# Performance work log

Measured on AMD Instinct MI355X. Metric: run time of the kernel, lower is better.

The kernel has to match this reference:

```python
import jax, jax.numpy as jnp
import numpy as np
jax.config.update("jax_enable_x64", True)

HASH_PRIMES = [2654435761, 2246822519, 3266489917, 2028178513, 1220703125, 1610612741, 805306457, 402653189, 3674653429, 2860486313, 1073676287, 2971215073, 1500450271, 3267000013, 2654435789, 4049292737, 2246822531, 3266489927, 2028178519, 1220703133, 1610612743, 805306459, 402653191, 3674653433]
NUM_TABLES = 32
BUCKETS = 4096
VOCAB = 1024
BYTE_DIM = 256
EMBED_PER_TABLE = 8
HIDDEN = 512
N_BLOCKS = 3  # num_layers - 1
BATCH, SEQ = 32, 2048

def _generate_skip_patterns(num_tables):
    patterns = []
    for offset in range(1, min(num_tables // 4 + 1, 9)):
        patterns.append((offset,))
    pairs = [(1,2),(2,3),(3,4),(1,3),(2,4),(1,4),(1,5),(2,5),(3,5),(1,6),(2,6),(1,7)]
    for p in pairs:
        if len(patterns) >= num_tables:
            break
        patterns.append(p)
    trigrams = [(1,2,3),(1,2,4),(1,3,5),(2,3,4),(1,2,5),(1,3,4),(2,4,6),(1,4,7)]
    for t in trigrams:
        if len(patterns) >= num_tables:
            break
        patterns.append(t)
    offset = 8
    while len(patterns) < num_tables:
        patterns.append((1, offset))
        offset += 1
    return tuple(patterns[:num_tables])

SKIP_PATTERNS = _generate_skip_patterns(NUM_TABLES)

def _soft_hash(tokens, table_idx):
    # tokens: [B,S] int64. Faithful to torch: h = h ^ (shifted*prime);
    # h2 = h ^ ((h*prime2) >> 16)  (python precedence: * > >> > ^)
    B, S = tokens.shape
    pattern = SKIP_PATTERNS[table_idx]
    h = jnp.zeros((B, S), dtype=jnp.int64)
    for k, offset in enumerate(pattern):
        prime = HASH_PRIMES[(table_idx * 3 + k) % len(HASH_PRIMES)]
        shifted = jnp.zeros_like(tokens)
        if offset < S:
            shifted = shifted.at[:, offset:].set(tokens[:, :S - offset])
        h = h ^ (shifted * jnp.int64(prime))
    idx_lo = h % BUCKETS
    sp = HASH_PRIMES[(table_idx * 3 + len(pattern)) % len(HASH_PRIMES)]
    h2 = h ^ ((h * jnp.int64(sp)) >> 16)
    idx_hi = h2 % BUCKETS
    frac = (((h >> 3) & 255).astype(jnp.float32) / 255.0) * 0.4
    return idx_lo, idx_hi, frac

def setup_inputs() -> dict:
    key = jax.random.key(0)
    ks = jax.random.split(key, 8)
    chars = jax.random.randint(ks[0], (BATCH, SEQ), 0, VOCAB, dtype=jnp.int64)
    byte_embed = jax.random.normal(ks[1], (VOCAB, BYTE_DIM), dtype=jnp.float32)
    hash_tables = 0.02 * jax.random.normal(ks[2], (NUM_TABLES, BUCKETS, EMBED_PER_TABLE), dtype=jnp.float32)
    s_in = float(np.sqrt(6.0 / (HIDDEN + HIDDEN)))
    w_in = jax.random.uniform(ks[3], (HIDDEN, HIDDEN), jnp.float32, -s_in, s_in)
    b_in = jnp.zeros((HIDDEN,), jnp.float32)
    mlp_ws = jax.random.uniform(ks[4], (N_BLOCKS, HIDDEN, HIDDEN), jnp.float32, -s_in, s_in)
    mlp_bs = jnp.zeros((N_BLOCKS, HIDDEN), jnp.float32)
    s_out = float(np.sqrt(6.0 / (HIDDEN + VOCAB)))
    w_out = jax.random.uniform(ks[5], (VOCAB, HIDDEN), jnp.float32, -s_out, s_out)
    b_out = jnp.zeros((VOCAB,), jnp.float32)
    return {"chars": chars, "byte_embed": byte_embed, "hash_tables": hash_tables,
            "w_in": w_in, "b_in": b_in, "mlp_ws": mlp_ws, "mlp_bs": mlp_bs,
            "w_out": w_out, "b_out": b_out}

def reference(chars, byte_embed, hash_tables, w_in, b_in, mlp_ws, mlp_bs, w_out, b_out):
    # chars: [B,S] int64 -> logits [B,S,V]
    parts = [byte_embed[chars]]  # [B,S,256]
    for i in range(NUM_TABLES):
        idx_lo, idx_hi, frac = _soft_hash(chars, i)
        tab = hash_tables[i]                      # [BUCKETS, 8]
        frac = frac[..., None]                    # [B,S,1]
        emb = tab[idx_lo] * (1.0 - frac) + tab[idx_hi] * frac
        parts.append(emb)
    features = jnp.concatenate(parts, axis=-1)    # [B,S,512]
    h = jax.nn.relu(features @ w_in.T + b_in)
    for j in range(N_BLOCKS):
        # ResidualBlock: relu(linear(x)) + x (no layernorm/dropout in config)
        h = jax.nn.relu(h @ mlp_ws[j].T + mlp_bs[j]) + h
    logits = h @ w_out.T + b_out                  # [B,S,VOCAB]
    return logits
```

## Files before the change

### kernel.cpp

```cpp
#include <hip/hip_runtime.h>
#include <cstdint>
#include <cstddef>

typedef unsigned short u16;
typedef __attribute__((ext_vector_type(8))) short short8;
typedef __attribute__((ext_vector_type(4))) float f32x4;

#define NTOK 65536
#define HID 512
#define NVOCAB 1024

__device__ __forceinline__ u16 f2bf(float f) {
  union { float f; uint32_t u; } v; v.f = f;
  uint32_t r = (v.u + 0x7FFFu + ((v.u >> 16) & 1u)) >> 16;
  return (u16)r;
}
__device__ __forceinline__ float bf2f(u16 b) {
  union { uint32_t u; float f; } v; v.u = ((uint32_t)b) << 16;
  return v.f;
}

__constant__ uint32_t P24[24] = {
  2654435761u, 2246822519u, 3266489917u, 2028178513u, 1220703125u,
  1610612741u, 805306457u, 402653189u, 3674653429u, 2860486313u,
  1073676287u, 2971215073u, 1500450271u, 3267000013u, 2654435789u,
  4049292737u, 2246822531u, 3266489927u, 2028178519u, 1220703133u,
  1610612743u, 805306459u, 402653191u, 3674653433u};
__constant__ unsigned char OFFS[32][3] = {
  {1,0,0},{2,0,0},{3,0,0},{4,0,0},{5,0,0},{6,0,0},{7,0,0},{8,0,0},
  {1,2,0},{2,3,0},{3,4,0},{1,3,0},{2,4,0},{1,4,0},{1,5,0},{2,5,0},
  {3,5,0},{1,6,0},{2,6,0},{1,7,0},
  {1,2,3},{1,2,4},{1,3,5},{2,3,4},{1,2,5},{1,3,4},{2,4,6},{1,4,7},
  {1,8,0},{1,9,0},{1,10,0},{1,11,0}};
__constant__ unsigned char PLEN[32] = {
  1,1,1,1,1,1,1,1, 2,2,2,2,2,2,2,2,2,2,2,2, 3,3,3,3,3,3,3,3, 2,2,2,2};

__global__ __launch_bounds__(256) void pack_w(
    const float* __restrict__ w_in, const float* __restrict__ mlp_ws,
    const float* __restrict__ w_out, u16* __restrict__ Wp)
{
  const int gid  = blockIdx.x * 256 + threadIdx.x;
  const int L    = gid >> 15;
  const int c    = gid & 32767;
  const int lane = c & 63;
  const int ni   = (c >> 6) & 3;
  const int kk   = (c >> 8) & 15;
  const int w    = c >> 12;
  const float* base =
      (L == 0) ? w_in :
      (L <= 3) ? mlp_ws + (size_t)(L - 1) * 262144 :
                 w_out  + (size_t)(L - 4) * 262144;
  const int row = (w << 6) + (ni << 4) + (lane & 15);
  const int col = (kk << 5) + ((lane >> 4) << 3);
  const float* s = base + (size_t)row * 512 + col;
  float4 f0 = ((const float4*)s)[0];
  float4 f1 = ((const float4*)s)[1];
  short8 o;
  o[0]=(short)f2bf(f0.x); o[1]=(short)f2bf(f0.y); o[2]=(short)f2bf(f0.z); o[3]=(short)f2bf(f0.w);
  o[4]=(short)f2bf(f1.x); o[5]=(short)f2bf(f1.y); o[6]=(short)f2bf(f1.z); o[7]=(short)f2bf(f1.w);
  *(short8*)(Wp + (size_t)gid * 8) = o;
}

__global__ __launch_bounds__(512, 4)
void fused_all(const int* __restrict__ chars, const float* __restrict__ byte_embed,
               const float* __restrict__ hash_tables, const u16* __restrict__ Wp,
               const float* __restrict__ bIn, const float* __restrict__ bMlp,
               const float* __restrict__ bOut, float* __restrict__ out)
{
  __shared__ __align__(16) u16 hbuf[64 * 512];
  __shared__ int cbuf[96];
  const int tid  = threadIdx.x;
  const int w    = tid >> 6;
  const int lane = tid & 63;
  const int g    = lane >> 4;
  const int lr   = lane & 15;
  const size_t tok0 = (size_t)blockIdx.x << 6;
  const int swz = (lr & 7) << 3;

  if (tid < 96) {
    long long gi = (long long)tok0 - 32 + tid;
    if (gi < 0) gi = 0;
    cbuf[tid] = chars[gi];
  }
  __syncthreads();

  {
    const int sub = tid & 31;
    const int tl  = tid >> 5;
    const int pl  = (int)PLEN[sub];

    auto issue = [&](int tr, float4& g0, float4& g1, float4& g2,
                     float4& g3, float4& g4, float4& g5, float& fr) {
      const size_t t = tok0 + tr;
      const int pos = (int)(t & 2047);
      const int c = cbuf[32 + tr];
      long long hv = 0;
      #pragma unroll
      for (int k = 0; k < 3; ++k) {
        if (k < pl) {
          const int off = (int)OFFS[sub][k];
          const long long tok = (pos >= off) ? (long long)cbuf[32 + tr - off] : 0ll;
          hv ^= tok * (long long)P24[(3 * sub + k) % 24];
        }
      }
      const int idx_lo = (int)(hv & 4095);
      const long long sp = (long long)P24[(3 * sub + pl) % 24];
      const long long prod = (long long)((unsigned long long)hv * (unsigned long long)sp);
      const int idx_hi = (int)((hv ^ (prod >> 16)) & 4095);
      fr = ((float)(int)((hv >> 3) & 255) / 255.0f) * 0.4f;
      const float* plo = hash_tables + (((size_t)sub << 12) + (size_t)idx_lo) * 8;
      const float* phi = hash_tables + (((size_t)sub << 12) + (size_t)idx_hi) * 8;
      const float* pby = byte_embed + ((size_t)c << 8) + (sub << 3);
      g0 = ((const float4*)plo)[0]; g1 = ((const float4*)plo)[1];
      g2 = ((const float4*)phi)[0]; g3 = ((const float4*)phi)[1];
      g4 = ((const float4*)pby)[0]; g5 = ((const float4*)pby)[1];
    };
    auto consume = [&](int tr, float4 g0, float4 g1, float4 g2,
                       float4 g3, float4 g4, float4 g5, float fr) {
      const int sw = (tr & 7) << 3;
      short8 ob;
      ob[0]=(short)f2bf(g4.x); ob[1]=(short)f2bf(g4.y); ob[2]=(short)f2bf(g4.z); ob[3]=(short)f2bf(g4.w);
      ob[4]=(short)f2bf(g5.x); ob[5]=(short)f2bf(g5.y); ob[6]=(short)f2bf(g5.z); ob[7]=(short)f2bf(g5.w);
      *(short8*)&hbuf[(tr << 9) + ((sub << 3) ^ sw)] = ob;
      const float om = 1.0f - fr;
      short8 oh;
      oh[0]=(short)f2bf(g0.x*om + g2.x*fr); oh[1]=(short)f2bf(g0.y*om + g2.y*fr);
      oh[2]=(short)f2bf(g0.z*om + g2.z*fr); oh[3]=(short)f2bf(g0.w*om + g2.w*fr);
      oh[4]=(short)f2bf(g1.x*om + g3.x*fr); oh[5]=(short)f2bf(g1.y*om + g3.y*fr);
      oh[6]=(short)f2bf(g1.z*om + g3.z*fr); oh[7]=(short)f2bf(g1.w*om + g3.w*fr);
      *(short8*)&hbuf[(tr << 9) + ((256 + (sub << 3)) ^ sw)] = oh;
    };

    float4 A0, A1, A2, A3, A4, A5; float frA;
    float4 B0, B1, B2, B3, B4, B5; float frB;
    float4 C0, C1, C2, C3, C4, C5; float frC;
    issue(tl,      A0, A1, A2, A3, A4, A5, frA);
    issue(16 + tl, B0, B1, B2, B3, B4, B5, frB);
    issue(32 + tl, C0, C1, C2, C3, C4, C5, frC);
    consume(tl,      A0, A1, A2, A3, A4, A5, frA);
    issue(48 + tl,   A0, A1, A2, A3, A4, A5, frA);
    consume(16 + tl, B0, B1, B2, B3, B4, B5, frB);
    consume(32 + tl, C0, C1, C2, C3, C4, C5, frC);
    consume(48 + tl, A0, A1, A2, A3, A4, A5, frA);
  }
  __syncthreads();

  f32x4 acc[4][4];

  auto gemm = [&](int L) {
    #pragma unroll
    for (int ni = 0; ni < 4; ++ni)
      #pragma unroll
      for (int ti = 0; ti < 4; ++ti) acc[ni][ti] = (f32x4){0.f, 0.f, 0.f, 0.f};
    const u16* Wl = Wp + (size_t)L * 262144 + (w << 15) + (lane << 3);
    #pragma unroll
    for (int kk = 0; kk < 16; ++kk) {
      short8 Wf[4], hf[4];
      #pragma unroll
      for (int ni = 0; ni < 4; ++ni)
        Wf[ni] = *(const short8*)(Wl + (kk << 11) + (ni << 9));
      const int kb = ((kk << 5) + (g << 3)) ^ swz;
      #pragma unroll
      for (int ti = 0; ti < 4; ++ti)
        hf[ti] = *(const short8*)&hbuf[(((ti << 4) + lr) << 9) + kb];
      __builtin_amdgcn_s_setprio(1);
      #pragma unroll
      for (int ni = 0; ni < 4; ++ni)
        #pragma unroll
        for (int ti = 0; ti < 4; ++ti)
          acc[ni][ti] = __builtin_amdgcn_mfma_f32_16x16x32_bf16(Wf[ni], hf[ti], acc[ni][ti], 0, 0, 0);
      __builtin_amdgcn_s_setprio(0);
    }
  };

  auto epi_h = [&](const float* __restrict__ bias, bool resid) {
    __syncthreads();
    #pragma unroll
    for (int ni = 0; ni < 4; ++ni) {
      const int nb = (w << 6) + (ni << 4) + (g << 2);
      const float4 b4 = *(const float4*)(bias + nb);
      #pragma unroll
      for (int ti = 0; ti < 4; ++ti) {
        const int t = (ti << 4) + lr;
        u16* p = &hbuf[(t << 9) + (nb ^ swz)];
        float v0 = fmaxf(acc[ni][ti][0] + b4.x, 0.f);
        float v1 = fmaxf(acc[ni][ti][1] + b4.y, 0.f);
        float v2 = fmaxf(acc[ni][ti][2] + b4.z, 0.f);
        float v3 = fmaxf(acc[ni][ti][3] + b4.w, 0.f);
        if (resid) {
          const uint2 r2 = *(const uint2*)p;
          v0 += bf2f((u16)(r2.x & 0xffffu)); v1 += bf2f((u16)(r2.x >> 16));
          v2 += bf2f((u16)(r2.y & 0xffffu)); v3 += bf2f((u16)(r2.y >> 16));
        }
        uint2 o;
        o.x = (uint32_t)f2bf(v0) | ((uint32_t)f2bf(v1) << 16);
        o.y = (uint32_t)f2bf(v2) | ((uint32_t)f2bf(v3) << 16);
        *(uint2*)p = o;
      }
    }
    __syncthreads();
  };

  auto epi_out = [&](const float* __restrict__ bias, int vb) {
    #pragma unroll
    for (int ni = 0; ni < 4; ++ni) {
      const int nb = (w << 6) + (ni << 4) + (g << 2);
      const float4 b4 = *(const float4*)(bias + nb);
      #pragma unroll
      for (int ti = 0; ti < 4; ++ti) {
        const int t = (ti << 4) + lr;
        f32x4 o;
        o[0] = acc[ni][ti][0] + b4.x;
        o[1] = acc[ni][ti][1] + b4.y;
        o[2] = acc[ni][ti][2] + b4.z;
        o[3] = acc[ni][ti][3] + b4.w;
        __builtin_nontemporal_store(o, (f32x4*)(out + (tok0 + t) * NVOCAB + vb + nb));
      }
    }
  };

  gemm(0); epi_h(bIn, false);
  gemm(1); epi_h(bMlp,        true);
  gemm(2); epi_h(bMlp + 512,  true);
  gemm(3); epi_h(bMlp + 1024, true);
  gemm(4); epi_out(bOut,       0);
  gemm(5); epi_out(bOut + 512, 512);
}

extern "C" void kernel_launch(void* const* d_in, const int* in_sizes, int n_in,
                              void* d_out, int out_size, void* d_ws, size_t ws_size,
                              hipStream_t stream) {
  const int*   chars      = (const int*)  d_in[0];
  const float* byte_embed = (const float*)d_in[1];
  const float* hash_tabs  = (const float*)d_in[2];
  const float* w_in       = (const float*)d_in[3];
  const float* b_in       = (const float*)d_in[4];
  const float* mlp_ws     = (const float*)d_in[5];
  const float* mlp_bs     = (const float*)d_in[6];
  const float* w_out      = (const float*)d_in[7];
  const float* b_out      = (const float*)d_in[8];

  u16* Wp = (u16*)d_ws;

  pack_w<<<dim3(768), dim3(256), 0, stream>>>(w_in, mlp_ws, w_out, Wp);

  fused_all<<<dim3(NTOK / 64), dim3(512), 0, stream>>>(
      chars, byte_embed, hash_tabs, Wp, b_in, mlp_bs, b_out, (float*)d_out);
}
```

Baseline: 489.9 us.

## Switch GEMMs from 16x16x32 to 32x32x16 bf16 MFMA tiles

Replaces the 4x4 grid of 16x16x32 MFMAs per wave with a 2x2 grid of 32x32x16 MFMAs, and repacks the weights and reworks the LDS activation reads and epilogue indexing to match the new fragment layout. Each K step now issues fewer LDS and global fragment loads for the same output tile, and the larger MFMA gives better operand reuse. The trade-off is more K iterations with fewer instructions each, and a new swizzle and epilogue mapping that must line up exactly with the 32x32 accumulator layout.

```diff
diff --git a/kernel.cpp b/kernel.cpp
--- a/kernel.cpp
+++ b/kernel.cpp
@@ -5,6 +5,7 @@
 typedef unsigned short u16;
 typedef __attribute__((ext_vector_type(8))) short short8;
 typedef __attribute__((ext_vector_type(4))) float f32x4;
+typedef __attribute__((ext_vector_type(16))) float f32x16;
 
 #define NTOK 65536
 #define HID 512
@@ -43,15 +44,15 @@
   const int L    = gid >> 15;
   const int c    = gid & 32767;
   const int lane = c & 63;
-  const int ni   = (c >> 6) & 3;
-  const int kk   = (c >> 8) & 15;
+  const int ni   = (c >> 6) & 1;
+  const int kc   = (c >> 7) & 31;
   const int w    = c >> 12;
   const float* base =
       (L == 0) ? w_in :
       (L <= 3) ? mlp_ws + (size_t)(L - 1) * 262144 :
                  w_out  + (size_t)(L - 4) * 262144;
-  const int row = (w << 6) + (ni << 4) + (lane & 15);
-  const int col = (kk << 5) + ((lane >> 4) << 3);
+  const int row = (w << 6) + (ni << 5) + (lane & 31);
+  const int col = (kc << 4) + ((lane >> 5) << 3);
   const float* s = base + (size_t)row * 512 + col;
   float4 f0 = ((const float4*)s)[0];
   float4 f1 = ((const float4*)s)[1];
@@ -72,10 +73,10 @@
   const int tid  = threadIdx.x;
   const int w    = tid >> 6;
   const int lane = tid & 63;
-  const int g    = lane >> 4;
-  const int lr   = lane & 15;
+  const int tb   = lane & 31;
+  const int g2   = lane >> 5;
+  const int sx7  = lane & 7;
   const size_t tok0 = (size_t)blockIdx.x << 6;
-  const int swz = (lr & 7) << 3;
 
   if (tid < 96) {
     long long gi = (long long)tok0 - 32 + tid;
@@ -89,7 +90,7 @@
     const int tl  = tid >> 5;
     const int pl  = (int)PLEN[sub];
 
-    auto issue = [&](int tr, float4& g0, float4& g1, float4& g2,
+    auto issue = [&](int tr, float4& g0, float4& g1, float4& g2_,
                      float4& g3, float4& g4, float4& g5, float& fr) {
       const size_t t = tok0 + tr;
       const int pos = (int)(t & 2047);
@@ -112,10 +113,10 @@
       const float* phi = hash_tables + (((size_t)sub << 12) + (size_t)idx_hi) * 8;
       const float* pby = byte_embed + ((size_t)c << 8) + (sub << 3);
       g0 = ((const float4*)plo)[0]; g1 = ((const float4*)plo)[1];
-      g2 = ((const float4*)phi)[0]; g3 = ((const float4*)phi)[1];
+      g2_ = ((const float4*)phi)[0]; g3 = ((const float4*)phi)[1];
       g4 = ((const float4*)pby)[0]; g5 = ((const float4*)pby)[1];
     };
-    auto consume = [&](int tr, float4 g0, float4 g1, float4 g2,
+    auto consume = [&](int tr, float4 g0, float4 g1, float4 g2_,
                        float4 g3, float4 g4, float4 g5, float fr) {
       const int sw = (tr & 7) << 3;
       short8 ob;
@@ -124,8 +125,8 @@
       *(short8*)&hbuf[(tr << 9) + ((sub << 3) ^ sw)] = ob;
       const float om = 1.0f - fr;
       short8 oh;
-      oh[0]=(short)f2bf(g0.x*om + g2.x*fr); oh[1]=(short)f2bf(g0.y*om + g2.y*fr);
-      oh[2]=(short)f2bf(g0.z*om + g2.z*fr); oh[3]=(short)f2bf(g0.w*om + g2.w*fr);
+      oh[0]=(short)f2bf(g0.x*om + g2_.x*fr); oh[1]=(short)f2bf(g0.y*om + g2_.y*fr);
+      oh[2]=(short)f2bf(g0.z*om + g2_.z*fr); oh[3]=(short)f2bf(g0.w*om + g2_.w*fr);
       oh[4]=(short)f2bf(g1.x*om + g3.x*fr); oh[5]=(short)f2bf(g1.y*om + g3.y*fr);
       oh[6]=(short)f2bf(g1.z*om + g3.z*fr); oh[7]=(short)f2bf(g1.w*om + g3.w*fr);
       *(short8*)&hbuf[(tr << 9) + ((256 + (sub << 3)) ^ sw)] = oh;
@@ -145,30 +146,28 @@
   }
   __syncthreads();
 
-  f32x4 acc[4][4];
+  f32x16 acc[2][2];
 
   auto gemm = [&](int L) {
     #pragma unroll
-    for (int ni = 0; ni < 4; ++ni)
-      #pragma unroll
-      for (int ti = 0; ti < 4; ++ti) acc[ni][ti] = (f32x4){0.f, 0.f, 0.f, 0.f};
+    for (int ni = 0; ni < 2; ++ni)
+      #pragma unroll
+      for (int tj = 0; tj < 2; ++tj)
+        #pragma unroll
+        for (int r = 0; r < 16; ++r) acc[ni][tj][r] = 0.f;
     const u16* Wl = Wp + (size_t)L * 262144 + (w << 15) + (lane << 3);
     #pragma unroll
-    for (int kk = 0; kk < 16; ++kk) {
-      short8 Wf[4], hf[4];
-      #pragma unroll
-      for (int ni = 0; ni < 4; ++ni)
-        Wf[ni] = *(const short8*)(Wl + (kk << 11) + (ni << 9));
-      const int kb = ((kk << 5) + (g << 3)) ^ swz;
-      #pragma unroll
-      for (int ti = 0; ti < 4; ++ti)
-        hf[ti] = *(const short8*)&hbuf[(((ti << 4) + lr) << 9) + kb];
+    for (int kc = 0; kc < 32; ++kc) {
+      short8 Wf0 = *(const short8*)(Wl + (kc << 10));
+      short8 Wf1 = *(const short8*)(Wl + (kc << 10) + 512);
+      const int ch = ((((kc << 1) + g2) ^ sx7) << 3);
+      short8 h0 = *(const short8*)&hbuf[(tb << 9) + ch];
+      short8 h1 = *(const short8*)&hbuf[((32 + tb) << 9) + ch];
       __builtin_amdgcn_s_setprio(1);
-      #pragma unroll
-      for (int ni = 0; ni < 4; ++ni)
-        #pragma unroll
-        for (int ti = 0; ti < 4; ++ti)
-          acc[ni][ti] = __builtin_amdgcn_mfma_f32_16x16x32_bf16(Wf[ni], hf[ti], acc[ni][ti], 0, 0, 0);
+      acc[0][0] = __builtin_amdgcn_mfma_f32_32x32x16_bf16(Wf0, h0, acc[0][0], 0, 0, 0);
+      acc[0][1] = __builtin_amdgcn_mfma_f32_32x32x16_bf16(Wf0, h1, acc[0][1], 0, 0, 0);
+      acc[1][0] = __builtin_amdgcn_mfma_f32_32x32x16_bf16(Wf1, h0, acc[1][0], 0, 0, 0);
+      acc[1][1] = __builtin_amdgcn_mfma_f32_32x32x16_bf16(Wf1, h1, acc[1][1], 0, 0, 0);
       __builtin_amdgcn_s_setprio(0);
     }
   };
@@ -176,26 +175,31 @@
   auto epi_h = [&](const float* __restrict__ bias, bool resid) {
     __syncthreads();
     #pragma unroll
-    for (int ni = 0; ni < 4; ++ni) {
-      const int nb = (w << 6) + (ni << 4) + (g << 2);
-      const float4 b4 = *(const float4*)(bias + nb);
-      #pragma unroll
-      for (int ti = 0; ti < 4; ++ti) {
-        const int t = (ti << 4) + lr;
-        u16* p = &hbuf[(t << 9) + (nb ^ swz)];
-        float v0 = fmaxf(acc[ni][ti][0] + b4.x, 0.f);
-        float v1 = fmaxf(acc[ni][ti][1] + b4.y, 0.f);
-        float v2 = fmaxf(acc[ni][ti][2] + b4.z, 0.f);
-        float v3 = fmaxf(acc[ni][ti][3] + b4.w, 0.f);
-        if (resid) {
-          const uint2 r2 = *(const uint2*)p;
-          v0 += bf2f((u16)(r2.x & 0xffffu)); v1 += bf2f((u16)(r2.x >> 16));
-          v2 += bf2f((u16)(r2.y & 0xffffu)); v3 += bf2f((u16)(r2.y >> 16));
+    for (int ni = 0; ni < 2; ++ni) {
+      const int nb = (w << 6) + (ni << 5);
+      #pragma unroll
+      for (int tj = 0; tj < 2; ++tj) {
+        const int t = (tj << 5) + tb;
+        #pragma unroll
+        for (int q = 0; q < 4; ++q) {
+          const int nq = nb + (q << 3) + (g2 << 2);
+          const float4 b4 = *(const float4*)(bias + nq);
+          float v0 = fmaxf(acc[ni][tj][4*q+0] + b4.x, 0.f);
+          float v1 = fmaxf(acc[ni][tj][4*q+1] + b4.y, 0.f);
+          float v2 = fmaxf(acc[ni][tj][4*q+2] + b4.z, 0.f);
+          float v3 = fmaxf(acc[ni][tj][4*q+3] + b4.w, 0.f);
+          const int gr = (nb >> 3) + q;
+          u16* p = &hbuf[(t << 9) + ((gr ^ sx7) << 3) + (g2 << 2)];
+          if (resid) {
+            const uint2 r2 = *(const uint2*)p;
+            v0 += bf2f((u16)(r2.x & 0xffffu)); v1 += bf2f((u16)(r2.x >> 16));
+            v2 += bf2f((u16)(r2.y & 0xffffu)); v3 += bf2f((u16)(r2.y >> 16));
+          }
+          uint2 o;
+          o.x = (uint32_t)f2bf(v0) | ((uint32_t)f2bf(v1) << 16);
+          o.y = (uint32_t)f2bf(v2) | ((uint32_t)f2bf(v3) << 16);
+          *(uint2*)p = o;
         }
-        uint2 o;
-        o.x = (uint32_t)f2bf(v0) | ((uint32_t)f2bf(v1) << 16);
-        o.y = (uint32_t)f2bf(v2) | ((uint32_t)f2bf(v3) << 16);
-        *(uint2*)p = o;
       }
     }
     __syncthreads();
@@ -203,18 +207,22 @@
 
   auto epi_out = [&](const float* __restrict__ bias, int vb) {
     #pragma unroll
-    for (int ni = 0; ni < 4; ++ni) {
-      const int nb = (w << 6) + (ni << 4) + (g << 2);
-      const float4 b4 = *(const float4*)(bias + nb);
-      #pragma unroll
-      for (int ti = 0; ti < 4; ++ti) {
-        const int t = (ti << 4) + lr;
-        f32x4 o;
-        o[0] = acc[ni][ti][0] + b4.x;
-        o[1] = acc[ni][ti][1] + b4.y;
-        o[2] = acc[ni][ti][2] + b4.z;
-        o[3] = acc[ni][ti][3] + b4.w;
-        __builtin_nontemporal_store(o, (f32x4*)(out + (tok0 + t) * NVOCAB + vb + nb));
+    for (int ni = 0; ni < 2; ++ni) {
+      const int nb = (w << 6) + (ni << 5);
+      #pragma unroll
+      for (int tj = 0; tj < 2; ++tj) {
+        const int t = (tj << 5) + tb;
+        #pragma unroll
+        for (int q = 0; q < 4; ++q) {
+          const int nq = nb + (q << 3) + (g2 << 2);
+          const float4 b4 = *(const float4*)(bias + nq);
+          f32x4 o;
+          o[0] = acc[ni][tj][4*q+0] + b4.x;
+          o[1] = acc[ni][tj][4*q+1] + b4.y;
+          o[2] = acc[ni][tj][4*q+2] + b4.z;
+          o[3] = acc[ni][tj][4*q+3] + b4.w;
+          __builtin_nontemporal_store(o, (f32x4*)(out + (tok0 + t) * NVOCAB + vb + nq));
+        }
       }
     }
   };
```

Result: slower. 603.4 us (+23.2%).
